# Kernel optimization log

Measured on AMD Instinct MI355X. Metric: run time of the kernel, lower is better.

Reference implementation:

```python
import jax, jax.numpy as jnp
import numpy as np

D_THRESH = 0.5  # init arg `dist`


def setup_inputs() -> dict:
    key = jax.random.key(0)
    k1, k2 = jax.random.split(key)
    N, M, C = 20000, 25000, 3
    pointcloud = jax.random.uniform(k1, (N, C), dtype=jnp.float32)
    pointcloud_padding = jax.random.uniform(k2, (M, C), dtype=jnp.float32)
    return {"pointcloud": pointcloud, "pointcloud_padding": pointcloud_padding}


def reference(pointcloud, pointcloud_padding):
    # torch.cdist(padding, pointcloud): Euclidean distance matrix [M, N]
    # via the GEMM formulation ||a||^2 + ||b||^2 - 2 a.b (matches torch's path)
    a2 = jnp.sum(pointcloud_padding * pointcloud_padding, axis=1)[:, None]  # [M,1]
    b2 = jnp.sum(pointcloud * pointcloud, axis=1)[None, :]                  # [1,N]
    ab = pointcloud_padding @ pointcloud.T                                  # [M,N]
    dist = jnp.sqrt(jnp.maximum(a2 + b2 - 2.0 * ab, 0.0))                   # [M,N]
    # count neighbors within radius, per pointcloud point
    counts = jnp.sum(dist <= D_THRESH, axis=0).astype(jnp.int32)            # [N]
    out = counts.reshape(-1, 1)[: pointcloud.shape[0]]                      # [N,1]
    return out
```

## Files before the change

kernel.cpp:

```cpp
#include <hip/hip_runtime.h>

typedef short  bf16x8 __attribute__((ext_vector_type(8)));

#define JS      13
#define STREAMS (JS * 4)
#define TI      64

__device__ __forceinline__ unsigned short f2bf(float x) {
    unsigned u = __builtin_bit_cast(unsigned, x);
    u += 0x7FFF + ((u >> 16) & 1);
    return (unsigned short)(u >> 16);
}
__device__ __forceinline__ float bf2f(unsigned short h) {
    unsigned u = ((unsigned)h) << 16;
    return __builtin_bit_cast(float, u);
}

__global__ __launch_bounds__(256) void dens_pack_kernel(
    const float* __restrict__ pad, uint4* __restrict__ ws,
    int* __restrict__ out, int M, int mtot, int N)
{
    const int j = blockIdx.x * 256 + threadIdx.x;
    if (j < N) out[j] = 0;
    if (j >= mtot) return;

    float qx = 0.f, qy = 0.f, qz = 0.f;
    float negc = -1.0e6f;
    if (j < M) {
        qx = pad[3 * j]; qy = pad[3 * j + 1]; qz = pad[3 * j + 2];
        negc = 0.125f - 0.5f * (qx * qx + qy * qy + qz * qz);
    }
    const unsigned short xh = f2bf(qx), yh = f2bf(qy), zh = f2bf(qz);
    const unsigned short xl = f2bf(qx - bf2f(xh));
    const unsigned short yl = f2bf(qy - bf2f(yh));
    const unsigned short zl = f2bf(qz - bf2f(zh));
    const unsigned short ch = f2bf(negc);
    const unsigned short cl = f2bf(negc - bf2f(ch));

    uint4 p0, p1;
    p0.x = (unsigned)xh | ((unsigned)yh << 16);
    p0.y = (unsigned)zh | ((unsigned)xl << 16);
    p0.z = (unsigned)yl | ((unsigned)zl << 16);
    p0.w = (unsigned)xh | ((unsigned)yh << 16);
    p1.x = (unsigned)zh | ((unsigned)xl << 16);
    p1.y = (unsigned)yl | ((unsigned)zl << 16);
    p1.z = (unsigned)ch | ((unsigned)cl << 16);
    p1.w = 0;
    ws[j]        = p0;
    ws[mtot + j] = p1;
}

__device__ __forceinline__ void make_bfrag(const float* __restrict__ pc,
                                           int i, int N, int half,
                                           bf16x8& B, float& nha)
{
    float px = 0.f, py = 0.f, pz = 0.f;
    float ha = 3.0e38f;
    if (i < N) {
        px = pc[3 * i]; py = pc[3 * i + 1]; pz = pc[3 * i + 2];
        ha = 0.5f * (px * px + py * py + pz * pz);
    }
    nha = -ha;
    const short xh = (short)f2bf(px), yh = (short)f2bf(py), zh = (short)f2bf(pz);
    const short xl = (short)f2bf(px - bf2f((unsigned short)xh));
    const short yl = (short)f2bf(py - bf2f((unsigned short)yh));
    const short zl = (short)f2bf(pz - bf2f((unsigned short)zh));
    const short ONE = (short)0x3F80;
    const bf16x8 B0 = {xh, yh, zh, xh, yh, zh, xl, yl};
    const bf16x8 B1 = {zl, xl, yl, zl, ONE, ONE, 0, 0};
    B = half ? B1 : B0;
}

#define CONS(R0,R1,R2,R3,R4,R5,R6,R7,R8,R9,RA,RB,RC,RD,RE,RF, CA, CB) \
    "v_ashrrev_i32 " R0 ", 31, " R0 "\n\t" \
    "v_ashrrev_i32 " R1 ", 31, " R1 "\n\t" \
    "v_ashrrev_i32 " R2 ", 31, " R2 "\n\t" \
    "v_ashrrev_i32 " R3 ", 31, " R3 "\n\t" \
    "v_ashrrev_i32 " R4 ", 31, " R4 "\n\t" \
    "v_ashrrev_i32 " R5 ", 31, " R5 "\n\t" \
    "v_ashrrev_i32 " R6 ", 31, " R6 "\n\t" \
    "v_ashrrev_i32 " R7 ", 31, " R7 "\n\t" \
    "v_ashrrev_i32 " R8 ", 31, " R8 "\n\t" \
    "v_ashrrev_i32 " R9 ", 31, " R9 "\n\t" \
    "v_ashrrev_i32 " RA ", 31, " RA "\n\t" \
    "v_ashrrev_i32 " RB ", 31, " RB "\n\t" \
    "v_ashrrev_i32 " RC ", 31, " RC "\n\t" \
    "v_ashrrev_i32 " RD ", 31, " RD "\n\t" \
    "v_ashrrev_i32 " RE ", 31, " RE "\n\t" \
    "v_ashrrev_i32 " RF ", 31, " RF "\n\t" \
    "v_add3_u32 " CA ", " R0 ", " R1 ", " CA "\n\t" \
    "v_add3_u32 " CB ", " R2 ", " R3 ", " CB "\n\t" \
    "v_add3_u32 " CA ", " R4 ", " R5 ", " CA "\n\t" \
    "v_add3_u32 " CB ", " R6 ", " R7 ", " CB "\n\t" \
    "v_add3_u32 " CA ", " R8 ", " R9 ", " CA "\n\t" \
    "v_add3_u32 " CB ", " RA ", " RB ", " CB "\n\t" \
    "v_add3_u32 " CA ", " RC ", " RD ", " CA "\n\t" \
    "v_add3_u32 " CB ", " RE ", " RF ", " CB "\n\t"

#define CONS_D0(CA, CB) \
    CONS("v32","v33","v34","v35","v36","v37","v38","v39", \
         "v40","v41","v42","v43","v44","v45","v46","v47", CA, CB)
#define CONS_D1(CA, CB) \
    CONS("v48","v49","v50","v51","v52","v53","v54","v55", \
         "v56","v57","v58","v59","v60","v61","v62","v63", CA, CB)

#define VISIT(AR, AD, ADLO, ADHI) \
    "s_waitcnt vmcnt(1)\n\t" \
    "v_mfma_f32_32x32x16_bf16 v[32:47], " AR ", %5, v[64:79]\n\t" \
    "v_mfma_f32_32x32x16_bf16 v[48:63], " AR ", %6, v[80:95]\n\t" \
    "global_load_dwordx4 " AR ", " AD ", off\n\t" \
    "v_add_co_u32 " ADLO ", vcc, 0xd000, " ADLO "\n\t" \
    "v_addc_co_u32 " ADHI ", vcc, 0, " ADHI ", vcc\n\t" \
    "s_nop 7\n\t" \
    "s_nop 2\n\t" \
    CONS_D0("%0", "%1") \
    CONS_D1("%2", "%3")

__global__ __launch_bounds__(256, 4) void dens_mfma_kernel(
    const float* __restrict__ pc,
    const char*  __restrict__ wsA,
    int* __restrict__ out,
    int N, int iters, int p1off)
{
    const int lane = threadIdx.x & 63;
    const int w    = threadIdx.x >> 6;
    const int n    = lane & 31;
    const int half = lane >> 5;

    const int ibase = blockIdx.x * TI;
    bf16x8 B0, B1; float nha0, nha1;
    make_bfrag(pc, ibase + n,      N, half, B0, nha0);
    make_bfrag(pc, ibase + 32 + n, N, half, B1, nha1);

    const int stream = blockIdx.y * 4 + w;
    const unsigned long long ax =
        (unsigned long long)(wsA + (half ? p1off : 0) + n * 16 + (size_t)stream * 512);
    const unsigned long long ay = ax + STREAMS * 512;
    const unsigned xlo = (unsigned)ax, xhi = (unsigned)(ax >> 32);
    const unsigned ylo = (unsigned)ay, yhi = (unsigned)(ay >> 32);

    int it = iters;
    int c0a = 0, c0b = 0, c1a = 0, c1b = 0;

    asm volatile(
        "v_mov_b32 v104, %9\n\t"
        "v_mov_b32 v105, %10\n\t"
        "v_mov_b32 v106, %11\n\t"
        "v_mov_b32 v107, %12\n\t"
        "v_mov_b32 v64, %7\n\t" "v_mov_b32 v65, %7\n\t"
        "v_mov_b32 v66, %7\n\t" "v_mov_b32 v67, %7\n\t"
        "v_mov_b32 v68, %7\n\t" "v_mov_b32 v69, %7\n\t"
        "v_mov_b32 v70, %7\n\t" "v_mov_b32 v71, %7\n\t"
        "v_mov_b32 v72, %7\n\t" "v_mov_b32 v73, %7\n\t"
        "v_mov_b32 v74, %7\n\t" "v_mov_b32 v75, %7\n\t"
        "v_mov_b32 v76, %7\n\t" "v_mov_b32 v77, %7\n\t"
        "v_mov_b32 v78, %7\n\t" "v_mov_b32 v79, %7\n\t"
        "v_mov_b32 v80, %8\n\t" "v_mov_b32 v81, %8\n\t"
        "v_mov_b32 v82, %8\n\t" "v_mov_b32 v83, %8\n\t"
        "v_mov_b32 v84, %8\n\t" "v_mov_b32 v85, %8\n\t"
        "v_mov_b32 v86, %8\n\t" "v_mov_b32 v87, %8\n\t"
        "v_mov_b32 v88, %8\n\t" "v_mov_b32 v89, %8\n\t"
        "v_mov_b32 v90, %8\n\t" "v_mov_b32 v91, %8\n\t"
        "v_mov_b32 v92, %8\n\t" "v_mov_b32 v93, %8\n\t"
        "v_mov_b32 v94, %8\n\t" "v_mov_b32 v95, %8\n\t"
        "global_load_dwordx4 v[96:99], v[104:105], off\n\t"
        "v_add_co_u32 v104, vcc, 0xd000, v104\n\t"
        "v_addc_co_u32 v105, vcc, 0, v105, vcc\n\t"
        "global_load_dwordx4 v[100:103], v[106:107], off\n\t"
        "v_add_co_u32 v106, vcc, 0xd000, v106\n\t"
        "v_addc_co_u32 v107, vcc, 0, v107, vcc\n\t"
        "Ldens%=:\n\t"
        VISIT("v[96:99]",  "v[104:105]", "v104", "v105")
        VISIT("v[100:103]","v[106:107]", "v106", "v107")
        "s_sub_u32 %4, %4, 1\n\t"
        "s_cmp_lg_u32 %4, 0\n\t"
        "s_cbranch_scc1 Ldens%=\n\t"
        : "+v"(c0a), "+v"(c0b), "+v"(c1a), "+v"(c1b), "+s"(it)
        : "v"(B0), "v"(B1), "v"(nha0), "v"(nha1),
          "v"(xlo), "v"(xhi), "v"(ylo), "v"(yhi)
        : "vcc", "scc", "memory",
          "v32","v33","v34","v35","v36","v37","v38","v39",
          "v40","v41","v42","v43","v44","v45","v46","v47",
          "v48","v49","v50","v51","v52","v53","v54","v55",
          "v56","v57","v58","v59","v60","v61","v62","v63",
          "v64","v65","v66","v67","v68","v69","v70","v71",
          "v72","v73","v74","v75","v76","v77","v78","v79",
          "v80","v81","v82","v83","v84","v85","v86","v87",
          "v88","v89","v90","v91","v92","v93","v94","v95",
          "v96","v97","v98","v99","v100","v101","v102","v103",
          "v104","v105","v106","v107");

    int t0 = c0a + c0b;  t0 += __shfl_xor(t0, 32);
    int t1 = c1a + c1b;  t1 += __shfl_xor(t1, 32);
    const int g0 = 512 + t0;
    const int g1 = 512 + t1;

    __shared__ int red[4][TI];
    if (lane < 32) { red[w][n] = g0; red[w][n + 32] = g1; }
    __syncthreads();
    if (threadIdx.x < TI) {
        const int ii = ibase + threadIdx.x;
        if (ii < N) {
            const int s = red[0][threadIdx.x] + red[1][threadIdx.x] +
                          red[2][threadIdx.x] + red[3][threadIdx.x];
            atomicAdd(&out[ii], s);
        }
    }
}

extern "C" void kernel_launch(void* const* d_in, const int* in_sizes, int n_in,
                              void* d_out, int out_size, void* d_ws, size_t ws_size,
                              hipStream_t stream) {
    const float* pc  = (const float*)d_in[0];
    const float* pad = (const float*)d_in[1];
    int* out = (int*)d_out;

    const int N = in_sizes[0] / 3;
    const int M = in_sizes[1] / 3;
    const int jt = (M + 31) / 32;
    int visits = (jt + STREAMS - 1) / STREAMS;
    if (visits & 1) visits++;
    const int jtp  = (visits + 2) * STREAMS;
    const int mtot = jtp * 32;

    dens_pack_kernel<<<(mtot + 255) / 256, 256, 0, stream>>>(
        pad, (uint4*)d_ws, out, M, mtot, N);

    dim3 grid((N + TI - 1) / TI, JS);
    dens_mfma_kernel<<<grid, 256, 0, stream>>>(
        pc, (const char*)d_ws, out, N, visits / 2, mtot * 16);
}
```

Before: 85.92 us.

## Widen block to 128 points and fold -|p|²/2 into the MFMA K dimension

Each block now handles 128 pointcloud points with four B fragments, so every loaded padding A-fragment feeds four MFMAs instead of two. The per-point -0.5|p|^2 bias moves out of the accumulator init and into the MFMA itself: the spare K slots now hold hi/lo bf16 copies of it, and the A pack sets those slots to 1.0. That allows a shared zero accumulator. Loads now use a single pointer stream with two buffers in flight, and the count base is computed from visits. This halves the number of blocks, which cuts A-fragment traffic and sign-count setup, but it risks lower occupancy or latency hiding and slight precision changes from the bf16 split of the bias.

Measured after the change: 85.57 us. No clear change (-0.4%).

```diff
diff --git a/kernel.cpp b/kernel.cpp
--- a/kernel.cpp
+++ b/kernel.cpp
@@ -4,7 +4,8 @@
 
 #define JS      13
 #define STREAMS (JS * 4)
-#define TI      64
+#define TI      128
+#define DEPTH   2
 
 __device__ __forceinline__ unsigned short f2bf(float x) {
     unsigned u = __builtin_bit_cast(unsigned, x);
@@ -45,14 +46,13 @@
     p1.x = (unsigned)zh | ((unsigned)xl << 16);
     p1.y = (unsigned)yl | ((unsigned)zl << 16);
     p1.z = (unsigned)ch | ((unsigned)cl << 16);
-    p1.w = 0;
+    p1.w = 0x3F803F80u;
     ws[j]        = p0;
     ws[mtot + j] = p1;
 }
 
 __device__ __forceinline__ void make_bfrag(const float* __restrict__ pc,
-                                           int i, int N, int half,
-                                           bf16x8& B, float& nha)
+                                           int i, int N, int half, bf16x8& B)
 {
     float px = 0.f, py = 0.f, pz = 0.f;
     float ha = 3.0e38f;
@@ -60,15 +60,17 @@
         px = pc[3 * i]; py = pc[3 * i + 1]; pz = pc[3 * i + 2];
         ha = 0.5f * (px * px + py * py + pz * pz);
     }
-    nha = -ha;
+    const float nha = -ha;
+    const unsigned short nhh = f2bf(nha);
+    const unsigned short nhl = f2bf(nha - bf2f(nhh));
     const short xh = (short)f2bf(px), yh = (short)f2bf(py), zh = (short)f2bf(pz);
     const short xl = (short)f2bf(px - bf2f((unsigned short)xh));
     const short yl = (short)f2bf(py - bf2f((unsigned short)yh));
     const short zl = (short)f2bf(pz - bf2f((unsigned short)zh));
     const short ONE = (short)0x3F80;
-    const bf16x8 B0 = {xh, yh, zh, xh, yh, zh, xl, yl};
-    const bf16x8 B1 = {zl, xl, yl, zl, ONE, ONE, 0, 0};
-    B = half ? B1 : B0;
+    const bf16x8 Blo = {xh, yh, zh, xh, yh, zh, xl, yl};
+    const bf16x8 Bhi = {zl, xl, yl, zl, ONE, ONE, (short)nhh, (short)nhl};
+    B = half ? Bhi : Blo;
 }
 
 #define CONS(R0,R1,R2,R3,R4,R5,R6,R7,R8,R9,RA,RB,RC,RD,RE,RF, CA, CB) \
@@ -104,23 +106,27 @@
     CONS("v48","v49","v50","v51","v52","v53","v54","v55", \
          "v56","v57","v58","v59","v60","v61","v62","v63", CA, CB)
 
-#define VISIT(AR, AD, ADLO, ADHI) \
+#define VISIT(AR) \
     "s_waitcnt vmcnt(1)\n\t" \
-    "v_mfma_f32_32x32x16_bf16 v[32:47], " AR ", %5, v[64:79]\n\t" \
-    "v_mfma_f32_32x32x16_bf16 v[48:63], " AR ", %6, v[80:95]\n\t" \
-    "global_load_dwordx4 " AR ", " AD ", off\n\t" \
-    "v_add_co_u32 " ADLO ", vcc, 0xd000, " ADLO "\n\t" \
-    "v_addc_co_u32 " ADHI ", vcc, 0, " ADHI ", vcc\n\t" \
+    "v_mfma_f32_32x32x16_bf16 v[32:47], " AR ", %9,  v[64:79]\n\t" \
+    "v_mfma_f32_32x32x16_bf16 v[48:63], " AR ", %10, v[64:79]\n\t" \
     "s_nop 7\n\t" \
     "s_nop 2\n\t" \
     CONS_D0("%0", "%1") \
-    CONS_D1("%2", "%3")
+    "v_mfma_f32_32x32x16_bf16 v[32:47], " AR ", %11, v[64:79]\n\t" \
+    CONS_D1("%2", "%3") \
+    "v_mfma_f32_32x32x16_bf16 v[48:63], " AR ", %12, v[64:79]\n\t" \
+    "global_load_dwordx4 " AR ", v[88:89], off\n\t" \
+    "v_add_co_u32 v88, vcc, 0x6800, v88\n\t" \
+    "v_addc_co_u32 v89, vcc, 0, v89, vcc\n\t" \
+    CONS_D0("%4", "%5") \
+    CONS_D1("%6", "%7")
 
 __global__ __launch_bounds__(256, 4) void dens_mfma_kernel(
     const float* __restrict__ pc,
     const char*  __restrict__ wsA,
     int* __restrict__ out,
-    int N, int iters, int p1off)
+    int N, int iters, int p1off, int visits)
 {
     const int lane = threadIdx.x & 63;
     const int w    = threadIdx.x >> 6;
@@ -128,56 +134,46 @@
     const int half = lane >> 5;
 
     const int ibase = blockIdx.x * TI;
-    bf16x8 B0, B1; float nha0, nha1;
-    make_bfrag(pc, ibase + n,      N, half, B0, nha0);
-    make_bfrag(pc, ibase + 32 + n, N, half, B1, nha1);
+    bf16x8 B0, B1, B2, B3;
+    make_bfrag(pc, ibase + n,      N, half, B0);
+    make_bfrag(pc, ibase + 32 + n, N, half, B1);
+    make_bfrag(pc, ibase + 64 + n, N, half, B2);
+    make_bfrag(pc, ibase + 96 + n, N, half, B3);
 
     const int stream = blockIdx.y * 4 + w;
     const unsigned long long ax =
         (unsigned long long)(wsA + (half ? p1off : 0) + n * 16 + (size_t)stream * 512);
-    const unsigned long long ay = ax + STREAMS * 512;
     const unsigned xlo = (unsigned)ax, xhi = (unsigned)(ax >> 32);
-    const unsigned ylo = (unsigned)ay, yhi = (unsigned)(ay >> 32);
 
     int it = iters;
-    int c0a = 0, c0b = 0, c1a = 0, c1b = 0;
+    int c0a = 0, c0b = 0, c1a = 0, c1b = 0, c2a = 0, c2b = 0, c3a = 0, c3b = 0;
 
     asm volatile(
-        "v_mov_b32 v104, %9\n\t"
-        "v_mov_b32 v105, %10\n\t"
-        "v_mov_b32 v106, %11\n\t"
-        "v_mov_b32 v107, %12\n\t"
-        "v_mov_b32 v64, %7\n\t" "v_mov_b32 v65, %7\n\t"
-        "v_mov_b32 v66, %7\n\t" "v_mov_b32 v67, %7\n\t"
-        "v_mov_b32 v68, %7\n\t" "v_mov_b32 v69, %7\n\t"
-        "v_mov_b32 v70, %7\n\t" "v_mov_b32 v71, %7\n\t"
-        "v_mov_b32 v72, %7\n\t" "v_mov_b32 v73, %7\n\t"
-        "v_mov_b32 v74, %7\n\t" "v_mov_b32 v75, %7\n\t"
-        "v_mov_b32 v76, %7\n\t" "v_mov_b32 v77, %7\n\t"
-        "v_mov_b32 v78, %7\n\t" "v_mov_b32 v79, %7\n\t"
-        "v_mov_b32 v80, %8\n\t" "v_mov_b32 v81, %8\n\t"
-        "v_mov_b32 v82, %8\n\t" "v_mov_b32 v83, %8\n\t"
-        "v_mov_b32 v84, %8\n\t" "v_mov_b32 v85, %8\n\t"
-        "v_mov_b32 v86, %8\n\t" "v_mov_b32 v87, %8\n\t"
-        "v_mov_b32 v88, %8\n\t" "v_mov_b32 v89, %8\n\t"
-        "v_mov_b32 v90, %8\n\t" "v_mov_b32 v91, %8\n\t"
-        "v_mov_b32 v92, %8\n\t" "v_mov_b32 v93, %8\n\t"
-        "v_mov_b32 v94, %8\n\t" "v_mov_b32 v95, %8\n\t"
-        "global_load_dwordx4 v[96:99], v[104:105], off\n\t"
-        "v_add_co_u32 v104, vcc, 0xd000, v104\n\t"
-        "v_addc_co_u32 v105, vcc, 0, v105, vcc\n\t"
-        "global_load_dwordx4 v[100:103], v[106:107], off\n\t"
-        "v_add_co_u32 v106, vcc, 0xd000, v106\n\t"
-        "v_addc_co_u32 v107, vcc, 0, v107, vcc\n\t"
+        "v_mov_b32 v88, %13\n\t"
+        "v_mov_b32 v89, %14\n\t"
+        "v_mov_b32 v64, 0\n\t" "v_mov_b32 v65, 0\n\t"
+        "v_mov_b32 v66, 0\n\t" "v_mov_b32 v67, 0\n\t"
+        "v_mov_b32 v68, 0\n\t" "v_mov_b32 v69, 0\n\t"
+        "v_mov_b32 v70, 0\n\t" "v_mov_b32 v71, 0\n\t"
+        "v_mov_b32 v72, 0\n\t" "v_mov_b32 v73, 0\n\t"
+        "v_mov_b32 v74, 0\n\t" "v_mov_b32 v75, 0\n\t"
+        "v_mov_b32 v76, 0\n\t" "v_mov_b32 v77, 0\n\t"
+        "v_mov_b32 v78, 0\n\t" "v_mov_b32 v79, 0\n\t"
+        "global_load_dwordx4 v[80:83], v[88:89], off\n\t"
+        "v_add_co_u32 v88, vcc, 0x6800, v88\n\t"
+        "v_addc_co_u32 v89, vcc, 0, v89, vcc\n\t"
+        "global_load_dwordx4 v[84:87], v[88:89], off\n\t"
+        "v_add_co_u32 v88, vcc, 0x6800, v88\n\t"
+        "v_addc_co_u32 v89, vcc, 0, v89, vcc\n\t"
         "Ldens%=:\n\t"
-        VISIT("v[96:99]",  "v[104:105]", "v104", "v105")
-        VISIT("v[100:103]","v[106:107]", "v106", "v107")
-        "s_sub_u32 %4, %4, 1\n\t"
-        "s_cmp_lg_u32 %4, 0\n\t"
+        VISIT("v[80:83]")
+        VISIT("v[84:87]")
+        "s_sub_u32 %8, %8, 1\n\t"
+        "s_cmp_lg_u32 %8, 0\n\t"
         "s_cbranch_scc1 Ldens%=\n\t"
-        : "+v"(c0a), "+v"(c0b), "+v"(c1a), "+v"(c1b), "+s"(it)
-        : "v"(B0), "v"(B1), "v"(nha0), "v"(nha1),
-          "v"(xlo), "v"(xhi), "v"(ylo), "v"(yhi)
+        : "+v"(c0a), "+v"(c0b), "+v"(c1a), "+v"(c1b),
+          "+v"(c2a), "+v"(c2b), "+v"(c3a), "+v"(c3b), "+s"(it)
+        : "v"(B0), "v"(B1), "v"(B2), "v"(B3), "v"(xlo), "v"(xhi)
         : "vcc", "scc", "memory",
           "v32","v33","v34","v35","v36","v37","v38","v39",
           "v40","v41","v42","v43","v44","v45","v46","v47",
@@ -186,17 +182,21 @@
           "v64","v65","v66","v67","v68","v69","v70","v71",
           "v72","v73","v74","v75","v76","v77","v78","v79",
           "v80","v81","v82","v83","v84","v85","v86","v87",
-          "v88","v89","v90","v91","v92","v93","v94","v95",
-          "v96","v97","v98","v99","v100","v101","v102","v103",
-          "v104","v105","v106","v107");
-
+          "v88","v89");
+
+    const int base = 32 * visits;
     int t0 = c0a + c0b;  t0 += __shfl_xor(t0, 32);
     int t1 = c1a + c1b;  t1 += __shfl_xor(t1, 32);
-    const int g0 = 512 + t0;
-    const int g1 = 512 + t1;
+    int t2 = c2a + c2b;  t2 += __shfl_xor(t2, 32);
+    int t3 = c3a + c3b;  t3 += __shfl_xor(t3, 32);
 
     __shared__ int red[4][TI];
-    if (lane < 32) { red[w][n] = g0; red[w][n + 32] = g1; }
+    if (lane < 32) {
+        red[w][n]      = base + t0;
+        red[w][n + 32] = base + t1;
+        red[w][n + 64] = base + t2;
+        red[w][n + 96] = base + t3;
+    }
     __syncthreads();
     if (threadIdx.x < TI) {
         const int ii = ibase + threadIdx.x;
@@ -220,7 +220,7 @@
     const int jt = (M + 31) / 32;
     int visits = (jt + STREAMS - 1) / STREAMS;
     if (visits & 1) visits++;
-    const int jtp  = (visits + 2) * STREAMS;
+    const int jtp  = (visits + DEPTH) * STREAMS;
     const int mtot = jtp * 32;
 
     dens_pack_kernel<<<(mtot + 255) / 256, 256, 0, stream>>>(
@@ -228,5 +228,5 @@
 
     dim3 grid((N + TI - 1) / TI, JS);
     dens_mfma_kernel<<<grid, 256, 0, stream>>>(
-        pc, (const char*)d_ws, out, N, visits / 2, mtot * 16);
-}
+        pc, (const char*)d_ws, out, N, visits / 2, mtot * 16, visits);
+}
```
